# Performance work log

Measured on AMD Instinct MI355X. Metric: run time of the kernel, lower is better.

The kernel has to match this reference:

```python
import jax, jax.numpy as jnp
import numpy as np

CODEBOOK_DIM = 512
CODEBOOK_SIZE = 1024
NUM_GROUPS = 8
D_GROUP = CODEBOOK_DIM // NUM_GROUPS  # 64


def setup_inputs() -> dict:
    key = jax.random.key(0)
    kx, kc = jax.random.split(key)
    x = jax.random.normal(kx, (8, 2048, CODEBOOK_DIM), dtype=jnp.float32)
    # kaiming_uniform_ per group: bound = sqrt(6 / fan_in), fan_in = D_GROUP
    bound = float(np.sqrt(6.0 / D_GROUP))
    codebook = jax.random.uniform(
        kc, (NUM_GROUPS, CODEBOOK_SIZE, D_GROUP),
        minval=-bound, maxval=bound, dtype=jnp.float32)
    return {"x": x, "codebook": codebook}


def reference(x, codebook):
    B, S, D = x.shape
    G, K, d = codebook.shape  # groups, codebook size, per-group dim
    xg = x.reshape(B, S, G, d)
    x_norm = jnp.sum(xg * xg, axis=-1, keepdims=True)          # [B,S,G,1]
    c_norm = jnp.sum(codebook * codebook, axis=-1)             # [G,K]
    cross = jnp.einsum('bsgd,gkd->bsgk', xg, codebook)         # [B,S,G,K]
    dist = x_norm + c_norm[None, None, :, :] - 2.0 * cross
    indices = jnp.argmin(dist, axis=-1)                        # [B,S,G]
    g_idx = jnp.arange(G)[None, None, :]                       # broadcast group ids
    quantized = codebook[g_idx, indices]                       # [B,S,G,d]
    quantized = quantized.reshape(B, S, D)
    # straight-through estimator: x + stop_grad(q - x)
    return x + jax.lax.stop_gradient(quantized - x)
```

## Files before the change

### kernel.cpp

```cpp
#include <hip/hip_runtime.h>


#define NTOK   16384
#define DMODEL 512
#define NGRP   8
#define DG     64
#define NCODE  1024
#define EPS    0.10f

typedef __attribute__((ext_vector_type(8))) __bf16 bf16x8;
typedef __attribute__((ext_vector_type(4))) float  f32x4;

__device__ __forceinline__ unsigned umin_(unsigned a, unsigned b){ return a<b?a:b; }
__device__ __forceinline__ unsigned umax_(unsigned a, unsigned b){ return a>b?a:b; }

__global__ __launch_bounds__(256) void prep_frags(
    const float* __restrict__ cb, __bf16* __restrict__ wb)
{
    int tid  = blockIdx.x * 256 + threadIdx.x;
    int lane = tid & 63;
    int s    = (tid >> 6) & 1;
    int ct   = (tid >> 7) & 63;
    int g    = tid >> 13;
    int code = ct * 16 + (lane & 15);
    int k0   = s * 32 + (lane >> 4) * 8;
    const float* src = cb + ((size_t)g * NCODE + code) * DG + k0;
    bf16x8 v;
    #pragma unroll
    for (int j = 0; j < 8; ++j) v[j] = (__bf16)src[j];
    *reinterpret_cast<bf16x8*>(wb + (size_t)tid * 8) = v;
}

__global__ __launch_bounds__(256) void prep_cnorm(
    const float* __restrict__ cb, float* __restrict__ wcn)
{
    int i = blockIdx.x * 256 + threadIdx.x;
    const float4* c4 = reinterpret_cast<const float4*>(cb + (size_t)i * DG);
    float s = 0.0f;
    #pragma unroll
    for (int j = 0; j < 16; ++j) {
        float4 v = c4[j];
        s = fmaf(v.x, v.x, s); s = fmaf(v.y, v.y, s);
        s = fmaf(v.z, v.z, s); s = fmaf(v.w, v.w, s);
    }
    wcn[i] = s;
}

__device__ __forceinline__ float dotc(const float* __restrict__ a,
                                      const float* __restrict__ b)
{
    const float4* a4 = reinterpret_cast<const float4*>(a);
    const float4* b4 = reinterpret_cast<const float4*>(b);
    float s = 0.0f;
    #pragma unroll 4
    for (int j = 0; j < 16; ++j) {
        float4 u = a4[j], v = b4[j];
        s = fmaf(u.x, v.x, s); s = fmaf(u.y, v.y, s);
        s = fmaf(u.z, v.z, s); s = fmaf(u.w, v.w, s);
    }
    return s;
}

__device__ __forceinline__ bf16x8 cvt8(const float* __restrict__ p)
{
    float4 u = *reinterpret_cast<const float4*>(p);
    float4 v = *reinterpret_cast<const float4*>(p + 4);
    bf16x8 r;
    r[0]=(__bf16)u.x; r[1]=(__bf16)u.y; r[2]=(__bf16)u.z; r[3]=(__bf16)u.w;
    r[4]=(__bf16)v.x; r[5]=(__bf16)v.y; r[6]=(__bf16)v.z; r[7]=(__bf16)v.w;
    return r;
}

__device__ __forceinline__ bf16x8 ldfrag(const __bf16* __restrict__ wbg,
                                         int ct, int shalf, int lane)
{
    return *reinterpret_cast<const bf16x8*>(
        wbg + ((size_t)(ct * 2 + shalf) * 64 + lane) * 8);
}

__global__ __launch_bounds__(256, 4) void vq_mfma_kernel(
    const float*  __restrict__ x,
    const float*  __restrict__ cb,
    const __bf16* __restrict__ wb,
    const float*  __restrict__ wcn,
    float* __restrict__ out)
{
    __shared__ float cn64[NCODE];

    const int tid  = threadIdx.x;
    const int lane = tid & 63;
    const int w    = tid >> 6;
    const int g    = blockIdx.x & 7;
    const int tile = blockIdx.x >> 3;

    {
        float4 v = reinterpret_cast<const float4*>(wcn + g * NCODE)[tid];
        v.x += 64.0f; v.y += 64.0f; v.z += 64.0f; v.w += 64.0f;
        reinterpret_cast<float4*>(cn64)[tid] = v;
    }
    __syncthreads();

    const int row  = lane & 15;
    const int q    = lane >> 4;
    const int k0   = q * 8;
    const int tok0 = tile * 128 + w * 32;

    bf16x8 aA[2], aB[2];
    #pragma unroll
    for (int s = 0; s < 2; ++s) {
        const float* xr = x + (size_t)(tok0 + s * 16 + row) * DMODEL + g * DG;
        aA[s] = cvt8(xr + k0);
        aB[s] = cvt8(xr + 32 + k0);
    }

    unsigned best[2][4], sec[2][4];
    #pragma unroll
    for (int s = 0; s < 2; ++s)
        #pragma unroll
        for (int r = 0; r < 4; ++r) { best[s][r] = 0xFFFFFFFFu; sec[s][r] = 0xFFFFFFFFu; }

    const __bf16* wbg = wb + (size_t)g * (NCODE * DG);

    bf16x8 b0a = ldfrag(wbg, 0, 0, lane), b1a = ldfrag(wbg, 0, 1, lane);
    bf16x8 b0b = ldfrag(wbg, 1, 0, lane), b1b = ldfrag(wbg, 1, 1, lane);

    for (int ct = 0; ct < 64; ct += 2) {
        {
            f32x4 d[2];
            #pragma unroll
            for (int s = 0; s < 2; ++s) {
                f32x4 z = {0.0f, 0.0f, 0.0f, 0.0f};
                z = __builtin_amdgcn_mfma_f32_16x16x32_bf16(aA[s], b0a, z, 0, 0, 0);
                d[s] = __builtin_amdgcn_mfma_f32_16x16x32_bf16(aB[s], b1a, z, 0, 0, 0);
            }
            const int nct = (ct + 2 < 64) ? (ct + 2) : 0;
            b0a = ldfrag(wbg, nct, 0, lane);
            b1a = ldfrag(wbg, nct, 1, lane);
            const int code = ct * 16 + row;
            const float cnv = cn64[code];
            #pragma unroll
            for (int s = 0; s < 2; ++s)
                #pragma unroll
                for (int r = 0; r < 4; ++r) {
                    float sd = fmaf(-2.0f, d[s][r], cnv);
                    unsigned key = (__float_as_uint(sd) & 0xFFFFFC00u) | (unsigned)code;
                    unsigned bo  = best[s][r];
                    best[s][r] = umin_(bo, key);
                    sec[s][r]  = umin_(sec[s][r], umax_(bo, key));
                }
        }
        {
            f32x4 d[2];
            #pragma unroll
            for (int s = 0; s < 2; ++s) {
                f32x4 z = {0.0f, 0.0f, 0.0f, 0.0f};
                z = __builtin_amdgcn_mfma_f32_16x16x32_bf16(aA[s], b0b, z, 0, 0, 0);
                d[s] = __builtin_amdgcn_mfma_f32_16x16x32_bf16(aB[s], b1b, z, 0, 0, 0);
            }
            const int nct = (ct + 3 < 64) ? (ct + 3) : 0;
            b0b = ldfrag(wbg, nct, 0, lane);
            b1b = ldfrag(wbg, nct, 1, lane);
            const int code = (ct + 1) * 16 + row;
            const float cnv = cn64[code];
            #pragma unroll
            for (int s = 0; s < 2; ++s)
                #pragma unroll
                for (int r = 0; r < 4; ++r) {
                    float sd = fmaf(-2.0f, d[s][r], cnv);
                    unsigned key = (__float_as_uint(sd) & 0xFFFFFC00u) | (unsigned)code;
                    unsigned bo  = best[s][r];
                    best[s][r] = umin_(bo, key);
                    sec[s][r]  = umin_(sec[s][r], umax_(bo, key));
                }
        }
    }

    unsigned mk[2][4];
    #pragma unroll
    for (int s = 0; s < 2; ++s)
        #pragma unroll
        for (int r = 0; r < 4; ++r) mk[s][r] = best[s][r];
    #pragma unroll
    for (int mask = 1; mask < 16; mask <<= 1) {
        #pragma unroll
        for (int s = 0; s < 2; ++s)
            #pragma unroll
            for (int r = 0; r < 4; ++r) {
                unsigned o = (unsigned)__shfl_xor((int)mk[s][r], mask, 64);
                mk[s][r] = umin_(mk[s][r], o);
            }
    }

    const float* cbg  = cb  + (size_t)g * NCODE * DG;
    const float* wcng = wcn + (size_t)g * NCODE;

    #pragma unroll
    for (int s = 0; s < 2; ++s) {
        #pragma unroll
        for (int r = 0; r < 4; ++r) {
            const unsigned m_ = mk[s][r];
            int sel = (int)(m_ & 0x3FFu);
            const float thr = __uint_as_float(m_ & 0xFFFFFC00u) + EPS;
            const float bd  = __uint_as_float(best[s][r] & 0xFFFFFC00u);
            const float sdd = __uint_as_float(sec[s][r]  & 0xFFFFFC00u);
            const bool oth = (bd <= thr && best[s][r] != m_) || (sdd <= thr);
            const unsigned long long bal = __ballot(oth);
            if (((bal >> (q * 16)) & 0xFFFFULL) != 0ULL) {
                const int token = tok0 + s * 16 + q * 4 + r;
                const float* xr = x + (size_t)token * DMODEL + g * DG;
                const float xn = dotc(xr, xr);
                float ed = 1e30f; int ei = 0x7FFFFFFF;
                if (bd <= thr) {
                    const int c = (int)(best[s][r] & 0x3FFu);
                    float dd = (xn + wcng[c]) - 2.0f * dotc(xr, cbg + (size_t)c * DG);
                    if (dd < ed || (dd == ed && c < ei)) { ed = dd; ei = c; }
                }
                if (sdd <= thr) {
                    const int c = (int)(sec[s][r] & 0x3FFu);
                    float dd = (xn + wcng[c]) - 2.0f * dotc(xr, cbg + (size_t)c * DG);
                    if (dd < ed || (dd == ed && c < ei)) { ed = dd; ei = c; }
                }
                #pragma unroll
                for (int mask = 1; mask < 16; mask <<= 1) {
                    float pd = __shfl_xor(ed, mask, 64);
                    int   pi = __shfl_xor(ei, mask, 64);
                    if (pd < ed || (pd == ed && pi < ei)) { ed = pd; ei = pi; }
                }
                sel = ei;
            }
            const int token = tok0 + s * 16 + q * 4 + r;
            const float4 src = reinterpret_cast<const float4*>(cbg + (size_t)sel * DG)[row];
            reinterpret_cast<float4*>(out + (size_t)token * DMODEL + g * DG)[row] = src;
        }
    }
}

__global__ __launch_bounds__(512, 4) void vq_fp32_kernel(
    const float* __restrict__ x,
    const float* __restrict__ cb,
    float* __restrict__ out)
{
    __shared__ float cnl[NGRP][NCODE];
    const int tid  = threadIdx.x;
    const int lane = tid & 63;
    const int wave = tid >> 6;
    const int g    = __builtin_amdgcn_readfirstlane(wave);
    const int token = blockIdx.x * 64 + lane;
    const float* __restrict__ cbg = cb + (size_t)g * NCODE * DG;

    for (int kk = lane; kk < NCODE; kk += 64) {
        const float4* c4 = reinterpret_cast<const float4*>(cbg + kk * DG);
        float s = 0.0f;
        #pragma unroll
        for (int j = 0; j < 16; ++j) {
            float4 v = c4[j];
            s = fmaf(v.x, v.x, s); s = fmaf(v.y, v.y, s);
            s = fmaf(v.z, v.z, s); s = fmaf(v.w, v.w, s);
        }
        cnl[g][kk] = s;
    }
    __syncthreads();

    const float* xr = x + (size_t)token * DMODEL + g * DG;
    float xn = dotc(xr, xr);
    float bestv = 3.4e38f; int bidx = 0;
    for (int k = 0; k < NCODE; ++k) {
        float dist = (xn + cnl[g][k]) - 2.0f * dotc(xr, cbg + (size_t)k * DG);
        if (dist < bestv) { bestv = dist; bidx = k; }
    }
    const float4* q4 = reinterpret_cast<const float4*>(cbg + (size_t)bidx * DG);
    float4* o4 = reinterpret_cast<float4*>(out + (size_t)token * DMODEL + g * DG);
    #pragma unroll
    for (int j = 0; j < 16; ++j) o4[j] = q4[j];
}

extern "C" void kernel_launch(void* const* d_in, const int* in_sizes, int n_in,
                              void* d_out, int out_size, void* d_ws, size_t ws_size,
                              hipStream_t stream) {
    const float* x  = (const float*)d_in[0];
    const float* cb = (const float*)d_in[1];
    float* out = (float*)d_out;

    const size_t wb_bytes = (size_t)NGRP * NCODE * DG * sizeof(__bf16);
    const size_t cn_bytes = (size_t)NGRP * NCODE * sizeof(float);
    if (ws_size < wb_bytes + cn_bytes) {
        vq_fp32_kernel<<<256, 512, 0, stream>>>(x, cb, out);
        return;
    }
    __bf16* wb  = (__bf16*)d_ws;
    float*  wcn = (float*)((char*)d_ws + wb_bytes);

    prep_frags<<<256, 256, 0, stream>>>(cb, wb);
    prep_cnorm<<<32, 256, 0, stream>>>(cb, wcn);
    vq_mfma_kernel<<<1024, 256, 0, stream>>>(x, cb, wb, wcn, out);
}
```

Measured before the change: 72.38 us.

## Stage codebook fragments in LDS with double-buffered async loads and fold norms into MFMA

Codebook bf16 fragments are now streamed into double-buffered shared memory with global_load_lds, in chunks of 256 codes, instead of each wave loading them from global memory. Blocks grow to 512 threads covering 256 tokens, so each chunk is shared by 8 waves. The -2 scale is folded into the prepared fragments and the code norm is fed in as the MFMA accumulator, which removes a per-element FMA. This cuts global/L2 traffic for the codebook, but it adds 64KB of LDS per block and a barrier per chunk, which may limit occupancy.

```diff
diff --git a/kernel.cpp b/kernel.cpp
--- a/kernel.cpp
+++ b/kernel.cpp
@@ -13,6 +13,12 @@
 
 __device__ __forceinline__ unsigned umin_(unsigned a, unsigned b){ return a<b?a:b; }
 __device__ __forceinline__ unsigned umax_(unsigned a, unsigned b){ return a>b?a:b; }
+
+__device__ __forceinline__ void gl_lds16(const void* g, void* l) {
+    __builtin_amdgcn_global_load_lds(
+        (const __attribute__((address_space(1))) unsigned int*)g,
+        (__attribute__((address_space(3))) unsigned int*)l, 16, 0, 0);
+}
 
 __global__ __launch_bounds__(256) void prep_frags(
     const float* __restrict__ cb, __bf16* __restrict__ wb)
@@ -27,7 +33,7 @@
     const float* src = cb + ((size_t)g * NCODE + code) * DG + k0;
     bf16x8 v;
     #pragma unroll
-    for (int j = 0; j < 8; ++j) v[j] = (__bf16)src[j];
+    for (int j = 0; j < 8; ++j) v[j] = (__bf16)(-2.0f * src[j]);
     *reinterpret_cast<bf16x8*>(wb + (size_t)tid * 8) = v;
 }
 
@@ -71,39 +77,44 @@
     return r;
 }
 
-__device__ __forceinline__ bf16x8 ldfrag(const __bf16* __restrict__ wbg,
-                                         int ct, int shalf, int lane)
-{
-    return *reinterpret_cast<const bf16x8*>(
-        wbg + ((size_t)(ct * 2 + shalf) * 64 + lane) * 8);
-}
-
-__global__ __launch_bounds__(256, 4) void vq_mfma_kernel(
+#define CHUNK_ELEM 16384
+
+__global__ __launch_bounds__(512, 4) void vq_mfma_kernel(
     const float*  __restrict__ x,
     const float*  __restrict__ cb,
     const __bf16* __restrict__ wb,
     const float*  __restrict__ wcn,
     float* __restrict__ out)
 {
-    __shared__ float cn64[NCODE];
+    __shared__ __bf16 bbuf[2][CHUNK_ELEM];
+    __shared__ float  cn64[NCODE];
 
     const int tid  = threadIdx.x;
     const int lane = tid & 63;
-    const int w    = tid >> 6;
+    const int wv   = tid >> 6;
     const int g    = blockIdx.x & 7;
     const int tile = blockIdx.x >> 3;
 
+    const __bf16* wbg = wb + (size_t)g * (NCODE * DG);
+
     {
-        float4 v = reinterpret_cast<const float4*>(wcn + g * NCODE)[tid];
-        v.x += 64.0f; v.y += 64.0f; v.z += 64.0f; v.w += 64.0f;
-        reinterpret_cast<float4*>(cn64)[tid] = v;
-    }
-    __syncthreads();
+        const __bf16* gsrc = wbg;
+        #pragma unroll
+        for (int i = 0; i < 4; ++i)
+            gl_lds16(gsrc + (size_t)(i * 512 + tid) * 8,
+                     (char*)&bbuf[0][0] + wv * 1024 + i * 8192);
+    }
+
+    {
+        float2 v = reinterpret_cast<const float2*>(wcn + g * NCODE)[tid];
+        float2 o; o.x = v.x + 64.0f; o.y = v.y + 64.0f;
+        reinterpret_cast<float2*>(cn64)[tid] = o;
+    }
 
     const int row  = lane & 15;
     const int q    = lane >> 4;
     const int k0   = q * 8;
-    const int tok0 = tile * 128 + w * 32;
+    const int tok0 = tile * 256 + wv * 32;
 
     bf16x8 aA[2], aB[2];
     #pragma unroll
@@ -119,60 +130,40 @@
         #pragma unroll
         for (int r = 0; r < 4; ++r) { best[s][r] = 0xFFFFFFFFu; sec[s][r] = 0xFFFFFFFFu; }
 
-    const __bf16* wbg = wb + (size_t)g * (NCODE * DG);
-
-    bf16x8 b0a = ldfrag(wbg, 0, 0, lane), b1a = ldfrag(wbg, 0, 1, lane);
-    bf16x8 b0b = ldfrag(wbg, 1, 0, lane), b1b = ldfrag(wbg, 1, 1, lane);
-
-    for (int ct = 0; ct < 64; ct += 2) {
-        {
-            f32x4 d[2];
+    __syncthreads();
+
+    for (int c = 0; c < 4; ++c) {
+        const int buf = c & 1;
+        if (c < 3) {
+            const __bf16* gsrc = wbg + (size_t)(c + 1) * CHUNK_ELEM;
+            #pragma unroll
+            for (int i = 0; i < 4; ++i)
+                gl_lds16(gsrc + (size_t)(i * 512 + tid) * 8,
+                         (char*)&bbuf[buf ^ 1][0] + wv * 1024 + i * 8192);
+        }
+        const __bf16* bb = &bbuf[buf][0];
+        #pragma unroll
+        for (int ctl = 0; ctl < 16; ++ctl) {
+            bf16x8 b0 = *reinterpret_cast<const bf16x8*>(bb + (ctl * 128 + lane) * 8);
+            bf16x8 b1 = *reinterpret_cast<const bf16x8*>(bb + (ctl * 128 + 64 + lane) * 8);
+            const int ct   = c * 16 + ctl;
+            const int code = ct * 16 + row;
+            const float cnv = cn64[code];
+            const f32x4 ci = {cnv, cnv, cnv, cnv};
             #pragma unroll
             for (int s = 0; s < 2; ++s) {
-                f32x4 z = {0.0f, 0.0f, 0.0f, 0.0f};
-                z = __builtin_amdgcn_mfma_f32_16x16x32_bf16(aA[s], b0a, z, 0, 0, 0);
-                d[s] = __builtin_amdgcn_mfma_f32_16x16x32_bf16(aB[s], b1a, z, 0, 0, 0);
-            }
-            const int nct = (ct + 2 < 64) ? (ct + 2) : 0;
-            b0a = ldfrag(wbg, nct, 0, lane);
-            b1a = ldfrag(wbg, nct, 1, lane);
-            const int code = ct * 16 + row;
-            const float cnv = cn64[code];
-            #pragma unroll
-            for (int s = 0; s < 2; ++s)
+                f32x4 z = __builtin_amdgcn_mfma_f32_16x16x32_bf16(aA[s], b0, ci, 0, 0, 0);
+                f32x4 d = __builtin_amdgcn_mfma_f32_16x16x32_bf16(aB[s], b1, z, 0, 0, 0);
                 #pragma unroll
                 for (int r = 0; r < 4; ++r) {
-                    float sd = fmaf(-2.0f, d[s][r], cnv);
-                    unsigned key = (__float_as_uint(sd) & 0xFFFFFC00u) | (unsigned)code;
+                    unsigned key = (__float_as_uint(d[r]) & 0xFFFFFC00u) | (unsigned)code;
                     unsigned bo  = best[s][r];
                     best[s][r] = umin_(bo, key);
                     sec[s][r]  = umin_(sec[s][r], umax_(bo, key));
                 }
-        }
-        {
-            f32x4 d[2];
-            #pragma unroll
-            for (int s = 0; s < 2; ++s) {
-                f32x4 z = {0.0f, 0.0f, 0.0f, 0.0f};
-                z = __builtin_amdgcn_mfma_f32_16x16x32_bf16(aA[s], b0b, z, 0, 0, 0);
-                d[s] = __builtin_amdgcn_mfma_f32_16x16x32_bf16(aB[s], b1b, z, 0, 0, 0);
             }
-            const int nct = (ct + 3 < 64) ? (ct + 3) : 0;
-            b0b = ldfrag(wbg, nct, 0, lane);
-            b1b = ldfrag(wbg, nct, 1, lane);
-            const int code = (ct + 1) * 16 + row;
-            const float cnv = cn64[code];
-            #pragma unroll
-            for (int s = 0; s < 2; ++s)
-                #pragma unroll
-                for (int r = 0; r < 4; ++r) {
-                    float sd = fmaf(-2.0f, d[s][r], cnv);
-                    unsigned key = (__float_as_uint(sd) & 0xFFFFFC00u) | (unsigned)code;
-                    unsigned bo  = best[s][r];
-                    best[s][r] = umin_(bo, key);
-                    sec[s][r]  = umin_(sec[s][r], umax_(bo, key));
-                }
-        }
+        }
+        __syncthreads();
     }
 
     unsigned mk[2][4];
@@ -211,14 +202,14 @@
                 const float xn = dotc(xr, xr);
                 float ed = 1e30f; int ei = 0x7FFFFFFF;
                 if (bd <= thr) {
-                    const int c = (int)(best[s][r] & 0x3FFu);
-                    float dd = (xn + wcng[c]) - 2.0f * dotc(xr, cbg + (size_t)c * DG);
-                    if (dd < ed || (dd == ed && c < ei)) { ed = dd; ei = c; }
+                    const int cc = (int)(best[s][r] & 0x3FFu);
+                    float dd = (xn + wcng[cc]) - 2.0f * dotc(xr, cbg + (size_t)cc * DG);
+                    if (dd < ed || (dd == ed && cc < ei)) { ed = dd; ei = cc; }
                 }
                 if (sdd <= thr) {
-                    const int c = (int)(sec[s][r] & 0x3FFu);
-                    float dd = (xn + wcng[c]) - 2.0f * dotc(xr, cbg + (size_t)c * DG);
-                    if (dd < ed || (dd == ed && c < ei)) { ed = dd; ei = c; }
+                    const int cc = (int)(sec[s][r] & 0x3FFu);
+                    float dd = (xn + wcng[cc]) - 2.0f * dotc(xr, cbg + (size_t)cc * DG);
+                    if (dd < ed || (dd == ed && cc < ei)) { ed = dd; ei = cc; }
                 }
                 #pragma unroll
                 for (int mask = 1; mask < 16; mask <<= 1) {
@@ -292,5 +283,5 @@
 
     prep_frags<<<256, 256, 0, stream>>>(cb, wb);
     prep_cnorm<<<32, 256, 0, stream>>>(cb, wcn);
-    vq_mfma_kernel<<<1024, 256, 0, stream>>>(x, cb, wb, wcn, out);
-}
+    vq_mfma_kernel<<<512, 512, 0, stream>>>(x, cb, wb, wcn, out);
+}
```

Measured after the change: 234.8 us. 224% more time.
